# Performance work log

Measured on AMD Instinct MI355X. Metric: run time of the kernel, lower is better.

## Reference

```python
import jax, jax.numpy as jnp
import numpy as np
from itertools import product

SPATIAL1 = (41, 1600, 1408)  # (z,y,x) = grid[::-1] + [1,0,0]
NUM_BATCH = 2
BN_EPS = 1e-3

# ---------- numpy rulebook construction (spconv-style, done once on host) ----------

def _encode(c, shape):
    D, H, W = [int(v) for v in shape]
    return ((c[:, 0].astype(np.int64) * D + c[:, 1]) * H + c[:, 2]) * W + c[:, 3]

def _lookup(skeys, order, cand):
    pos = np.clip(np.searchsorted(skeys, cand), 0, len(skeys) - 1)
    hit = skeys[pos] == cand
    return hit, order[pos]

def _pad_rb(pairs, n_in, n_out):
    P = max(max(len(a) for a, _ in pairs), 1)
    K = len(pairs)
    ii = np.full((K, P), n_in, np.int32)   # sentinel -> zero feature row
    oo = np.full((K, P), n_out, np.int32)  # sentinel -> dummy output row
    for k, (a, b) in enumerate(pairs):
        ii[k, :len(a)] = a
        oo[k, :len(b)] = b
    return ii, oo

def _subm_rb(coords, shape):
    # SubMConv3d k=3 p=1 s=1: output sites == input sites
    N = len(coords)
    keys = _encode(coords, shape)
    order = np.argsort(keys); skeys = keys[order]
    dims = np.array(shape)
    pairs = []
    for off in product((-1, 0, 1), repeat=3):
        nb = coords[:, 1:] + np.array(off)
        ok = (nb >= 0).all(1) & (nb < dims).all(1)
        oid = np.nonzero(ok)[0]
        cand = _encode(np.concatenate([coords[ok, :1], nb[ok]], 1), shape)
        hit, iid = _lookup(skeys, order, cand)
        pairs.append((iid[hit].astype(np.int32), oid[hit].astype(np.int32)))
    return _pad_rb(pairs, N, N)

def _down_rb(coords, in_shape, ks, st, pd):
    # SparseConv3d: output site active iff any kernel tap hits an active input
    dims = np.array(in_shape); ks = np.array(ks); st = np.array(st); pd = np.array(pd)
    out_shape = (dims + 2 * pd - ks) // st + 1
    offs = list(product(*[range(int(k)) for k in ks]))
    outs = []
    for off in offs:
        o = coords[:, 1:] + pd - np.array(off)
        ok = (o % st == 0).all(1)
        od = o // st
        ok &= (od >= 0).all(1) & (od < out_shape).all(1)
        outs.append(np.concatenate([coords[ok, :1], od[ok]], 1))
    out_coords = np.unique(np.concatenate(outs, 0), axis=0)
    keys = _encode(coords, in_shape)
    order = np.argsort(keys); skeys = keys[order]
    pairs = []
    for off in offs:
        ic = out_coords[:, 1:] * st - pd + np.array(off)
        ok = (ic >= 0).all(1) & (ic < dims).all(1)
        oid = np.nonzero(ok)[0]
        cand = _encode(np.concatenate([out_coords[ok, :1], ic[ok]], 1), in_shape)
        hit, iid = _lookup(skeys, order, cand)
        pairs.append((iid[hit].astype(np.int32), oid[hit].astype(np.int32)))
    ii, oo = _pad_rb(pairs, len(coords), len(out_coords))
    return ii, oo, out_coords, tuple(int(v) for v in out_shape)

def _gen_coords(rng):
    # clustered LiDAR-like active voxels (surfaces -> local density)
    D, H, W = SPATIAL1
    per = []
    for b in range(NUM_BATCH):
        centers = rng.integers([3, 30, 30], [D - 4, H - 31, W - 31], size=(600, 3))
        pts = centers[:, None, :] + rng.integers(-3, 4, size=(600, 60, 3))
        pts = np.clip(pts.reshape(-1, 3), 0, np.array([D - 1, H - 1, W - 1]))
        uniq = np.unique(pts, axis=0)
        per.append(np.concatenate([np.full((len(uniq), 1), b, np.int64), uniq], 1))
    return np.concatenate(per, 0)

CHANS = [(27, 4, 16), (27, 16, 16), (27, 16, 32), (27, 32, 32), (27, 32, 32),
         (27, 32, 64), (27, 64, 64), (27, 64, 64), (27, 64, 64), (27, 64, 64),
         (27, 64, 64), (3, 64, 128)]

def setup_inputs() -> dict:
    rng = np.random.default_rng(0)
    coords = _gen_coords(rng)  # (N,4) [b,z,y,x]
    N = len(coords)
    s1i, s1o = _subm_rb(coords, SPATIAL1)
    d2i, d2o, c2, s2 = _down_rb(coords, SPATIAL1, (3, 3, 3), (2, 2, 2), (1, 1, 1))
    s2i, s2o = _subm_rb(c2, s2)
    d3i, d3o, c3, s3 = _down_rb(c2, s2, (3, 3, 3), (2, 2, 2), (1, 1, 1))
    s3i, s3o = _subm_rb(c3, s3)
    d4i, d4o, c4, s4 = _down_rb(c3, s3, (3, 3, 3), (2, 2, 2), (0, 1, 1))
    s4i, s4o = _subm_rb(c4, s4)
    oi, oo, c5, s5 = _down_rb(c4, s4, (3, 1, 1), (2, 1, 1), (0, 0, 0))

    key = jax.random.key(0)
    ks = jax.random.split(key, 40)
    inp = {}
    for i, (K, ci, co) in enumerate(CHANS):
        inp[f"w{i}"] = (jax.random.normal(ks[i], (K, ci, co), jnp.float32)
                         / np.sqrt(K * ci)).astype(jnp.float32)
        kb = jax.random.split(ks[12 + i], 4)
        inp[f"bn{i}"] = jnp.stack([
            jax.random.uniform(kb[0], (co,)) + 0.5,   # gamma
            jax.random.normal(kb[1], (co,)) * 0.1,    # beta
            jax.random.normal(kb[2], (co,)) * 0.1,    # running mean
            jax.random.uniform(kb[3], (co,)) + 0.5,   # running var
        ]).astype(jnp.float32)
    inp["voxels"] = jax.random.normal(ks[30], (N, 5, 4), jnp.float32)
    inp["voxel_num_points"] = jax.random.randint(ks[31], (N,), 0, 6).astype(jnp.int32)
    for name, arr in [("subm1_in", s1i), ("subm1_out", s1o), ("down2_in", d2i),
                      ("down2_out", d2o), ("subm2_in", s2i), ("subm2_out", s2o),
                      ("down3_in", d3i), ("down3_out", d3o), ("subm3_in", s3i),
                      ("subm3_out", s3o), ("down4_in", d4i), ("down4_out", d4o),
                      ("subm4_in", s4i), ("subm4_out", s4o), ("out_in", oi),
                      ("out_out", oo)]:
        inp[name] = jnp.asarray(arr)
    inp["batch_idx"] = jnp.asarray(c5[:, 0].astype(np.int32))
    inp["n2"] = len(c2); inp["n3"] = len(c3); inp["n4"] = len(c4); inp["n5"] = len(c5)
    inp["n_batch"] = NUM_BATCH
    return inp

# ---------- jax forward ----------

def _sconv(feats, w, in_idx, out_idx, n_out):
    # gather -> per-kernel-offset GEMM -> scatter-add (spconv implicit GEMM)
    fpad = jnp.concatenate([feats, jnp.zeros((1, feats.shape[1]), feats.dtype)], 0)
    g = fpad[in_idx]                                  # (K,P,Cin)
    contrib = jnp.einsum('kpi,kio->kpo', g, w)        # (K,P,Cout)
    out = jnp.zeros((n_out + 1, w.shape[2]), feats.dtype)
    return out.at[out_idx].add(contrib)[:n_out]

def _bnrelu(x, bn):
    g, b, m, v = bn  # eval-mode BatchNorm1d, eps=1e-3
    return jax.nn.relu((x - m) * jax.lax.rsqrt(v + BN_EPS) * g + b)

def reference(voxels, voxel_num_points, w0, w1, w2, w3, w4, w5, w6, w7, w8, w9,
              w10, w11, bn0, bn1, bn2, bn3, bn4, bn5, bn6, bn7, bn8, bn9, bn10,
              bn11, subm1_in, subm1_out, down2_in, down2_out, subm2_in, subm2_out,
              down3_in, down3_out, subm3_in, subm3_out, down4_in, down4_out,
              subm4_in, subm4_out, out_in, out_out, batch_idx, n2, n3, n4, n5,
              n_batch):
    # mean-VFE: average point features per voxel
    denom = jnp.maximum(voxel_num_points.astype(voxels.dtype), 1.0)[:, None]
    x = voxels.sum(1) / denom                              # (N,4)
    n1 = x.shape[0]
    x = _bnrelu(_sconv(x, w0, subm1_in, subm1_out, n1), bn0)   # conv_input
    x = _bnrelu(_sconv(x, w1, subm1_in, subm1_out, n1), bn1)   # conv1
    x = _bnrelu(_sconv(x, w2, down2_in, down2_out, n2), bn2)   # conv2 (s2)
    x = _bnrelu(_sconv(x, w3, subm2_in, subm2_out, n2), bn3)
    x = _bnrelu(_sconv(x, w4, subm2_in, subm2_out, n2), bn4)
    x = _bnrelu(_sconv(x, w5, down3_in, down3_out, n3), bn5)   # conv3 (s2)
    x = _bnrelu(_sconv(x, w6, subm3_in, subm3_out, n3), bn6)
    x = _bnrelu(_sconv(x, w7, subm3_in, subm3_out, n3), bn7)
    x = _bnrelu(_sconv(x, w8, down4_in, down4_out, n4), bn8)   # conv4 (s2)
    x = _bnrelu(_sconv(x, w9, subm4_in, subm4_out, n4), bn9)
    x = _bnrelu(_sconv(x, w10, subm4_in, subm4_out, n4), bn10)
    x = _bnrelu(_sconv(x, w11, out_in, out_out, n5), bn11)     # conv_out
    # dc_feats: per-sample global max pool over active voxels (== max_pool1d)
    dc = jax.ops.segment_max(x, batch_idx, num_segments=n_batch)
    return dc
```

## Files before the change

### kernel.cpp

```cpp
#include <hip/hip_runtime.h>

#define TPB 256
typedef unsigned short u16;
typedef __attribute__((ext_vector_type(8))) short short8v;
typedef __attribute__((ext_vector_type(4))) float f32x4;

__device__ __forceinline__ u16 f2bf(float x) {
    unsigned u = __float_as_uint(x);
    return (u16)((u + 0x7FFFu + ((u >> 16) & 1u)) >> 16);
}
__device__ __forceinline__ float bf2f(u16 h) {
    return __uint_as_float(((unsigned)h) << 16);
}

template<int CS>
__device__ __forceinline__ int swzc(int r, int c) {
    constexpr int PH = (CS == 8) ? 0 : 1;
    return c ^ ((r >> PH) & (CS - 1));
}

__device__ __forceinline__ int xcd_swz(int bid, int nwg) {
    int q = nwg >> 3, r = nwg & 7;
    int x = bid & 7, idx = bid >> 3;
    return (x < r ? x * (q + 1) : r * (q + 1) + (x - r) * q) + idx;
}

__device__ __forceinline__ void gld16(const u16* g, u16* l) {
    __builtin_amdgcn_global_load_lds(
        (const __attribute__((address_space(1))) void*)g,
        (__attribute__((address_space(3))) void*)l, 16, 0, 0);
}

__global__ void vfe_kernel(const float* __restrict__ voxels,
                           const int* __restrict__ nump,
                           float* __restrict__ x, int N) {
    int i = blockIdx.x * blockDim.x + threadIdx.x;
    if (i >= N * 4) return;
    int n = i >> 2, c = i & 3;
    const float* v = voxels + (long)n * 20 + c;
    float s = v[0] + v[4] + v[8] + v[12] + v[16];
    x[i] = s / fmaxf((float)nump[n], 1.0f);
}

struct IBE { const int* rin; const int* rout; int* inv; int P, K, n_in, n_out, KP; };
struct IBA { IBE e[8]; };
__global__ void inv_build_all_kernel(IBA a, long grand) {
    long t = (long)blockIdx.x * blockDim.x + threadIdx.x;
    if (t >= grand) return;
    #pragma unroll
    for (int i = 0; i < 8; ++i) {
        if (t < a.e[i].KP) {
            const IBE& E = a.e[i];
            int ii = E.rin[t];
            if (ii != E.n_in) {
                int k = (int)(t / E.P);
                E.inv[(long)k * E.n_out + E.rout[t]] = ii;
            }
            return;
        }
        t -= a.e[i].KP;
    }
}

struct WPE { const float* w; u16* oh; u16* ol; int K, ci, co, total, pci; };
struct WPA { WPE e[11]; };
__global__ void wprep_kernel(WPA a, long grand) {
    long t = (long)blockIdx.x * blockDim.x + threadIdx.x;
    if (t >= grand) return;
    #pragma unroll
    for (int i = 0; i < 11; ++i) {
        if (t < a.e[i].total) {
            const WPE& E = a.e[i];
            if (E.pci) {
                int ci2 = 2 * E.pci;
                int p = (int)(t / (E.co * ci2));
                int rem = (int)(t % (E.co * ci2));
                int o = rem / ci2, ci = rem % ci2;
                int tap = 2 * p + ci / E.pci;
                float x = (tap < 27)
                    ? E.w[((long)tap * E.pci + (ci % E.pci)) * E.co + o] : 0.f;
                u16 h = f2bf(x);
                float lf = x - bf2f(h);
                int cs = ci2 >> 3, ph = (cs == 8) ? 0 : 1;
                int ch = ci >> 3, e = ci & 7;
                int sch = ch ^ ((o >> ph) & (cs - 1));
                long d = ((long)p * E.co + o) * ci2 + sch * 8 + e;
                E.oh[d] = h; E.ol[d] = f2bf(lf);
            } else {
                int cc = E.ci * E.co;
                int k = (int)(t / cc), r = (int)(t % cc), c = r / E.co, o = r % E.co;
                float x = E.w[t];
                u16 h = f2bf(x);
                float lf = x - bf2f(h);
                int cs = E.ci >> 3, ph = (cs == 8) ? 0 : 1;
                int ch = c >> 3, e = c & 7;
                int sch = ch ^ ((o >> ph) & (cs - 1));
                long d = ((long)k * E.co + o) * E.ci + sch * 8 + e;
                E.oh[d] = h; E.ol[d] = f2bf(lf);
            }
            return;
        }
        t -= a.e[i].total;
    }
}

template<int CO, int K>
__global__ __launch_bounds__(256)
void dconv4_kernel(const float* __restrict__ feats,
                   const float* __restrict__ w,
                   const float* __restrict__ bn,
                   const int* __restrict__ inv, int inv_n,
                   u16* __restrict__ oh, u16* __restrict__ ol,
                   int n_out) {
    constexpr int OG = CO / 4;
    __shared__ float sW[K * 4 * CO];
    for (int i = threadIdx.x; i < K * 4 * CO; i += 256) sW[i] = w[i];
    __syncthreads();
    long t = (long)blockIdx.x * 256 + threadIdx.x;
    int row = (int)(t / OG), og = (int)(t % OG);
    if (row >= n_out) return;
    float a0 = 0.f, a1 = 0.f, a2 = 0.f, a3 = 0.f;
    for (int k = 0; k < K; ++k) {
        int idx = inv[(long)k * inv_n + row];
        if (idx < 0) continue;
        float4 av = *(const float4*)(feats + (long)idx * 4);
        const float* wk = sW + k * 4 * CO + og * 4;
        #pragma unroll
        for (int ci = 0; ci < 4; ++ci) {
            float a = (&av.x)[ci];
            a0 = fmaf(a, wk[ci * CO + 0], a0);
            a1 = fmaf(a, wk[ci * CO + 1], a1);
            a2 = fmaf(a, wk[ci * CO + 2], a2);
            a3 = fmaf(a, wk[ci * CO + 3], a3);
        }
    }
    float4 g = *(const float4*)(bn + og * 4);
    float4 b = *(const float4*)(bn + CO + og * 4);
    float4 m = *(const float4*)(bn + 2 * CO + og * 4);
    float4 v = *(const float4*)(bn + 3 * CO + og * 4);
    float o4[4];
    o4[0] = fmaxf((a0 - m.x) * rsqrtf(v.x + 1e-3f) * g.x + b.x, 0.f);
    o4[1] = fmaxf((a1 - m.y) * rsqrtf(v.y + 1e-3f) * g.y + b.y, 0.f);
    o4[2] = fmaxf((a2 - m.z) * rsqrtf(v.z + 1e-3f) * g.z + b.z, 0.f);
    o4[3] = fmaxf((a3 - m.w) * rsqrtf(v.w + 1e-3f) * g.w + b.w, 0.f);
    long base = (long)row * CO + og * 4;
    #pragma unroll
    for (int c = 0; c < 4; ++c) {
        u16 h = f2bf(o4[c]);
        oh[base + c] = h;
        ol[base + c] = f2bf(o4[c] - bf2f(h));
    }
}

template<int CI, int CO, int KPt, int KT, bool PAIRED, int PCI, int EPI>
__global__ __launch_bounds__(256, 4)
void mconv_kernel(const u16* __restrict__ fh, const u16* __restrict__ fl,
                  const u16* __restrict__ wh, const u16* __restrict__ wl,
                  const int* __restrict__ inv,
                  const u16* __restrict__ zpage,
                  float* __restrict__ part, long slab_elems,
                  const float* __restrict__ bn,
                  u16* __restrict__ oh, u16* __restrict__ ol,
                  float* __restrict__ outf,
                  int n_out, int kpb) {
    constexpr int CS  = CI / 8;
    constexpr int LCS = (CS == 8) ? 3 : 2;
    constexpr int PH  = (CS == 8) ? 0 : 1;
    constexpr int KS  = CI / 32;
    constexpr int WC  = (CO >= 32) ? 2 : 1;
    constexpr int MT  = (WC == 2) ? 2 : 1;
    constexpr int NTW = CO / (16 * WC);
    constexpr int ASL = 64 * CS;
    constexpr int BSL = CO * CS;
    constexpr int AIT = (ASL + 255) / 256;
    constexpr int BIT = (BSL + 255) / 256;
    constexpr int SUBCS = PAIRED ? (PCI / 8) : 1;

    __shared__ __align__(16) u16 sAh[64 * CI];
    __shared__ __align__(16) u16 sAl[64 * CI];
    __shared__ __align__(16) u16 sBh[CO * CI];
    __shared__ __align__(16) u16 sBl[CO * CI];

    const int t = threadIdx.x;
    const int bx = xcd_swz(blockIdx.x, gridDim.x);
    const int brow = bx * 64;
    const int kbeg = blockIdx.y * kpb;
    const int kend = (kbeg + kpb < KPt) ? (kbeg + kpb) : KPt;

    const int lane = t & 63, wid = t >> 6;
    const int wr = wid / WC, wc = wid % WC;
    const int frow = lane & 15;
    const int fch  = lane >> 4;

    f32x4 acc[MT][NTW];
    #pragma unroll
    for (int mt = 0; mt < MT; ++mt)
        #pragma unroll
        for (int nt = 0; nt < NTW; ++nt) {
            acc[mt][nt][0] = 0.f; acc[mt][nt][1] = 0.f;
            acc[mt][nt][2] = 0.f; acc[mt][nt][3] = 0.f;
        }

    auto stage = [&](int k) {
        #pragma unroll
        for (int s = 0; s < AIT; ++s) {
            int slot = s * 256 + t;
            if (ASL % 256 == 0 || slot < ASL) {
                int r = slot >> LCS, cc = slot & (CS - 1);
                int c = cc ^ ((r >> PH) & (CS - 1));
                int grow = brow + r;
                const u16 *srcH, *srcL;
                if (PAIRED) {
                    int tap = 2 * k + c / SUBCS;
                    int within = c % SUBCS;
                    int idx = (grow < n_out && tap < KT)
                              ? inv[(long)tap * n_out + grow] : -1;
                    srcH = (idx >= 0) ? fh + (long)idx * PCI + within * 8 : zpage;
                    srcL = (idx >= 0) ? fl + (long)idx * PCI + within * 8 : zpage;
                } else {
                    int idx = (grow < n_out) ? inv[(long)k * n_out + grow] : -1;
                    srcH = (idx >= 0) ? fh + (long)idx * CI + c * 8 : zpage;
                    srcL = (idx >= 0) ? fl + (long)idx * CI + c * 8 : zpage;
                }
                gld16(srcH, sAh + (s * 256 + wid * 64) * 8);
                gld16(srcL, sAl + (s * 256 + wid * 64) * 8);
            }
        }
        const u16* gbh = wh + (long)k * CO * CI;
        const u16* gbl = wl + (long)k * CO * CI;
        #pragma unroll
        for (int s = 0; s < BIT; ++s) {
            int slot = s * 256 + t;
            if (BSL % 256 == 0 || slot < BSL) {
                gld16(gbh + (long)slot * 8, sBh + (s * 256 + wid * 64) * 8);
                gld16(gbl + (long)slot * 8, sBl + (s * 256 + wid * 64) * 8);
            }
        }
    };
    auto compute = [&]() {
        #pragma unroll
        for (int ks = 0; ks < KS; ++ks) {
            int c = ks * 4 + fch;
            short8v ah[MT], al[MT];
            #pragma unroll
            for (int mt = 0; mt < MT; ++mt) {
                int r = wr * (MT * 16) + mt * 16 + frow;
                int o = r * CI + swzc<CS>(r, c) * 8;
                ah[mt] = *(const short8v*)(sAh + o);
                al[mt] = *(const short8v*)(sAl + o);
            }
            #pragma unroll
            for (int nt = 0; nt < NTW; ++nt) {
                int col = wc * (CO / WC) + nt * 16 + frow;
                int o = col * CI + swzc<CS>(col, c) * 8;
                short8v bh = *(const short8v*)(sBh + o);
                short8v bl = *(const short8v*)(sBl + o);
                #pragma unroll
                for (int mt = 0; mt < MT; ++mt) {
                    acc[mt][nt] = __builtin_amdgcn_mfma_f32_16x16x32_bf16(ah[mt], bh, acc[mt][nt], 0, 0, 0);
                    acc[mt][nt] = __builtin_amdgcn_mfma_f32_16x16x32_bf16(ah[mt], bl, acc[mt][nt], 0, 0, 0);
                    acc[mt][nt] = __builtin_amdgcn_mfma_f32_16x16x32_bf16(al[mt], bh, acc[mt][nt], 0, 0, 0);
                }
            }
        }
    };

    for (int k = kbeg; k < kend; ++k) {
        stage(k);
        __syncthreads();
        compute();
        if (k + 1 < kend) __syncthreads();
    }

    if constexpr (EPI == 0) {
        float* dst = part + (long)blockIdx.y * slab_elems;
        #pragma unroll
        for (int mt = 0; mt < MT; ++mt) {
            int orow0 = brow + wr * (MT * 16) + mt * 16 + (lane >> 4) * 4;
            #pragma unroll
            for (int nt = 0; nt < NTW; ++nt) {
                int ocol = wc * (CO / WC) + nt * 16 + (lane & 15);
                #pragma unroll
                for (int j = 0; j < 4; ++j) {
                    int r = orow0 + j;
                    if (r < n_out) dst[(long)r * CO + ocol] = acc[mt][nt][j];
                }
            }
        }
    } else {
        #pragma unroll
        for (int mt = 0; mt < MT; ++mt) {
            int orow0 = brow + wr * (MT * 16) + mt * 16 + (lane >> 4) * 4;
            #pragma unroll
            for (int nt = 0; nt < NTW; ++nt) {
                int ocol = wc * (CO / WC) + nt * 16 + (lane & 15);
                float g = bn[ocol], bb = bn[CO + ocol];
                float m = bn[2 * CO + ocol], vv = bn[3 * CO + ocol];
                float sc = rsqrtf(vv + 1e-3f) * g;
                #pragma unroll
                for (int j = 0; j < 4; ++j) {
                    int r = orow0 + j;
                    if (r < n_out) {
                        float yv = fmaxf((acc[mt][nt][j] - m) * sc + bb, 0.f);
                        if constexpr (EPI == 1) {
                            u16 h = f2bf(yv);
                            oh[(long)r * CO + ocol] = h;
                            ol[(long)r * CO + ocol] = f2bf(yv - bf2f(h));
                        } else {
                            outf[(long)r * CO + ocol] = yv;
                        }
                    }
                }
            }
        }
    }
}

template<bool EMIT16>
__global__ void reduce_bnrelu_kernel(const float* __restrict__ part, long stride,
                                     int ys, const float* __restrict__ bn, int co,
                                     float* __restrict__ outf,
                                     u16* __restrict__ oh, u16* __restrict__ ol,
                                     long total4) {
    long t4 = (long)blockIdx.x * blockDim.x + threadIdx.x;
    if (t4 >= total4) return;
    long base = t4 * 4;
    float4 s = make_float4(0.f, 0.f, 0.f, 0.f);
    for (int y = 0; y < ys; ++y) {
        float4 v = *(const float4*)(part + (long)y * stride + base);
        s.x += v.x; s.y += v.y; s.z += v.z; s.w += v.w;
    }
    int o = (int)(base % co);
    float4 g = *(const float4*)(bn + o);
    float4 b = *(const float4*)(bn + co + o);
    float4 m = *(const float4*)(bn + 2 * co + o);
    float4 v = *(const float4*)(bn + 3 * co + o);
    float y0 = fmaxf((s.x - m.x) * rsqrtf(v.x + 1e-3f) * g.x + b.x, 0.f);
    float y1 = fmaxf((s.y - m.y) * rsqrtf(v.y + 1e-3f) * g.y + b.y, 0.f);
    float y2 = fmaxf((s.z - m.z) * rsqrtf(v.z + 1e-3f) * g.z + b.z, 0.f);
    float y3 = fmaxf((s.w - m.w) * rsqrtf(v.w + 1e-3f) * g.w + b.w, 0.f);
    if (EMIT16) {
        u16 h0 = f2bf(y0), h1 = f2bf(y1), h2 = f2bf(y2), h3 = f2bf(y3);
        ushort4 hv = { h0, h1, h2, h3 };
        ushort4 lv = { f2bf(y0 - bf2f(h0)), f2bf(y1 - bf2f(h1)),
                       f2bf(y2 - bf2f(h2)), f2bf(y3 - bf2f(h3)) };
        *(ushort4*)(oh + base) = hv;
        *(ushort4*)(ol + base) = lv;
    } else {
        *(float4*)(outf + base) = make_float4(y0, y1, y2, y3);
    }
}

__global__ void segmax_kernel(const float* __restrict__ x,
                              const int* __restrict__ bidx,
                              float* __restrict__ out, int rows, int nb) {
    __shared__ float sM[8 * 128];
    for (int i = threadIdx.x; i < nb * 128; i += 256) sM[i] = 0.f;
    __syncthreads();
    int c = threadIdx.x & 127;
    int sub = threadIdx.x >> 7;
    for (int r = blockIdx.x * 2 + sub; r < rows; r += gridDim.x * 2) {
        float v = x[(long)r * 128 + c];
        int b = bidx[r];
        atomicMax((int*)&sM[b * 128 + c], __float_as_int(v));
    }
    __syncthreads();
    for (int i = threadIdx.x; i < nb * 128; i += 256)
        atomicMax((int*)out + i, __float_as_int(sM[i]));
}

extern "C" void kernel_launch(void* const* d_in, const int* in_sizes, int n_in,
                              void* d_out, int out_size, void* d_ws, size_t ws_size,
                              hipStream_t stream) {
    (void)n_in;
    const float* voxels = (const float*)d_in[24];
    const int*   nump   = (const int*)d_in[25];
    const int N  = in_sizes[25];
    const int n2 = in_sizes[30] / 27;
    const int n3 = in_sizes[34] / 27;
    const int n4 = in_sizes[38] / 27;
    const int n5 = in_sizes[42];

    struct L { int wi, rb, K, ci, co, nin, nout; };
    const L layers[12] = {
        {0,  26, 27,  4,  16, N,  N }, {1,  26, 27, 16,  16, N,  N },
        {2,  28, 27, 16,  32, N,  n2}, {3,  30, 27, 32,  32, n2, n2},
        {4,  30, 27, 32,  32, n2, n2}, {5,  32, 27, 32,  64, n2, n3},
        {6,  34, 27, 64,  64, n3, n3}, {7,  34, 27, 64,  64, n3, n3},
        {8,  36, 27, 64,  64, n3, n4}, {9,  38, 27, 64,  64, n4, n4},
        {10, 38, 27, 64,  64, n4, n4}, {11, 40,  3, 64, 128, n4, n5},
    };
    struct RBD { int rb, K, nin, nout; };
    const RBD rbs[8] = {
        {26, 27, N,  N }, {28, 27, N,  n2}, {30, 27, n2, n2}, {32, 27, n2, n3},
        {34, 27, n3, n3}, {36, 27, n3, n4}, {38, 27, n4, n4}, {40, 3,  n4, n5},
    };
    const int invmap[12] = {0, 0, 1, 2, 2, 3, 4, 4, 5, 6, 6, 7};

    size_t feat_elems = (size_t)N * 4, wst_elems = 0, arena_elems = 0;
    size_t wst_off[12];
    for (int i = 0; i < 12; ++i) {
        size_t fe = (size_t)layers[i].nout * layers[i].co;
        if (fe > feat_elems) feat_elems = fe;
        if (i >= 5) { wst_off[i] = wst_elems;
                      wst_elems += (size_t)layers[i].K * layers[i].ci * layers[i].co; }
    }
    for (int r = 0; r < 8; ++r) arena_elems += (size_t)rbs[r].nout * rbs[r].K;
    const int pair_pci[4] = {16, 16, 32, 32};
    const int pair_co[4]  = {16, 32, 32, 32};
    size_t wpd_elems[4], wpd_off[4], wpd_tot = 0;
    for (int j = 0; j < 4; ++j) {
        wpd_elems[j] = (size_t)14 * pair_co[j] * 2 * pair_pci[j];
        wpd_off[j] = wpd_tot; wpd_tot += wpd_elems[j];
    }
    auto al = [](size_t x) { return (x + 255) & ~(size_t)255; };
    char* p = (char*)d_ws;
    u16*   zpage = (u16*)p; p += 256;
    int*   inv_arena = (int*)p; p += al(arena_elems * 4);
    float* bufA = (float*)p; p += al(feat_elems * 4);
    u16* ph[2]; u16* pl[2];
    ph[0] = (u16*)p; p += al(feat_elems * 2);
    pl[0] = (u16*)p; p += al(feat_elems * 2);
    ph[1] = (u16*)p; p += al(feat_elems * 2);
    pl[1] = (u16*)p; p += al(feat_elems * 2);
    u16* wth = (u16*)p; p += al(wst_elems * 2);
    u16* wtl = (u16*)p; p += al(wst_elems * 2);
    u16* wph = (u16*)p; p += al(wpd_tot * 2);
    u16* wpl = (u16*)p; p += al(wpd_tot * 2);
    float* slab = (float*)p;
    size_t slab_budget = ws_size - (size_t)((char*)slab - (char*)d_ws);

    hipMemsetAsync(zpage, 0, 256, stream);

    int* invs[8];
    {
        size_t off = 0;
        for (int r = 0; r < 8; ++r) { invs[r] = inv_arena + off; off += (size_t)rbs[r].nout * rbs[r].K; }
        hipMemsetAsync(inv_arena, 0xFF, arena_elems * sizeof(int), stream);
        IBA ia;
        long grand = 0;
        for (int r = 0; r < 8; ++r) {
            int P  = in_sizes[rbs[r].rb] / rbs[r].K;
            ia.e[r].rin  = (const int*)d_in[rbs[r].rb];
            ia.e[r].rout = (const int*)d_in[rbs[r].rb + 1];
            ia.e[r].inv  = invs[r];
            ia.e[r].P = P; ia.e[r].K = rbs[r].K; ia.e[r].n_in = rbs[r].nin;
            ia.e[r].n_out = rbs[r].nout;
            ia.e[r].KP = rbs[r].K * P;
            grand += ia.e[r].KP;
        }
        inv_build_all_kernel<<<dim3((unsigned)((grand + TPB - 1) / TPB)), dim3(TPB), 0, stream>>>(ia, grand);
    }

    {
        long tot = (long)N * 4;
        vfe_kernel<<<dim3((unsigned)((tot + TPB - 1) / TPB)), dim3(TPB), 0, stream>>>(
            voxels, nump, bufA, N);
    }

    {
        WPA wa;
        long grand = 0;
        for (int i = 5; i < 12; ++i) {
            const L& l = layers[i];
            WPE& E = wa.e[i - 5];
            E.w  = (const float*)d_in[2 * l.wi];
            E.oh = wth + wst_off[i];
            E.ol = wtl + wst_off[i];
            E.K = l.K; E.ci = l.ci; E.co = l.co;
            E.total = l.K * l.ci * l.co;
            E.pci = 0;
            grand += E.total;
        }
        for (int j = 0; j < 4; ++j) {
            WPE& E = wa.e[7 + j];
            E.w  = (const float*)d_in[2 * layers[1 + j].wi];
            E.oh = wph + wpd_off[j];
            E.ol = wpl + wpd_off[j];
            E.K = 27; E.ci = pair_pci[j]; E.co = pair_co[j];
            E.total = (int)wpd_elems[j];
            E.pci = pair_pci[j];
            grand += E.total;
        }
        wprep_kernel<<<dim3((unsigned)((grand + TPB - 1) / TPB)), dim3(TPB), 0, stream>>>(wa, grand);
    }

    {
        const L& l = layers[0];
        long tot = (long)l.nout * 4;
        dconv4_kernel<16, 27><<<dim3((unsigned)((tot + 255) / 256)), 256, 0, stream>>>(
            bufA, (const float*)d_in[0], (const float*)d_in[1], invs[0], l.nout,
            ph[0], pl[0], l.nout);
    }

    int cset = 0;
    for (int i = 1; i < 12; ++i) {
        const L& l = layers[i];
        const int* invp = invs[invmap[i]];
        unsigned blocks = (unsigned)((l.nout + 63) / 64);
        int KPv = (i <= 4) ? 14 : l.K;
        int ysmax = (KPv == 14) ? 9 : ((KPv == 27) ? 27 : 3);
        size_t per = (size_t)l.nout * l.co * 4;
        int ys = 1;
        while (ys < ysmax && blocks * (unsigned)ys < 768) ys *= 3;
        if (ys > ysmax) ys = ysmax;
        while (ys > 1 && (size_t)ys * per > slab_budget) ys /= 3;
        int kpb = (KPv + ys - 1) / ys;
        long slab_elems = (long)l.nout * l.co;
        dim3 grid(blocks, (unsigned)ys);
        const float* bn = (const float*)d_in[2 * l.wi + 1];
        const u16* fh = ph[cset];
        const u16* fl = pl[cset];
        const u16* whp = (i >= 5) ? wth + wst_off[i] : wph + wpd_off[i - 1];
        const u16* wlp = (i >= 5) ? wtl + wst_off[i] : wpl + wpd_off[i - 1];

        #define MCONV(CI_, CO_, KP_, KT_, PRD_, PCI_)                                  \
            do {                                                                       \
                if (ys == 1 && i < 11)                                                 \
                    mconv_kernel<CI_, CO_, KP_, KT_, PRD_, PCI_, 1><<<grid, 256, 0, stream>>>( \
                        fh, fl, whp, wlp, invp, zpage, nullptr, 0, bn,                 \
                        ph[cset ^ 1], pl[cset ^ 1], nullptr, l.nout, kpb);             \
                else if (ys == 1)                                                      \
                    mconv_kernel<CI_, CO_, KP_, KT_, PRD_, PCI_, 2><<<grid, 256, 0, stream>>>( \
                        fh, fl, whp, wlp, invp, zpage, nullptr, 0, bn,                 \
                        nullptr, nullptr, bufA, l.nout, kpb);                          \
                else                                                                   \
                    mconv_kernel<CI_, CO_, KP_, KT_, PRD_, PCI_, 0><<<grid, 256, 0, stream>>>( \
                        fh, fl, whp, wlp, invp, zpage, slab, slab_elems, bn,           \
                        nullptr, nullptr, nullptr, l.nout, kpb);                       \
            } while (0)

        switch (i) {
        case 1:          MCONV(32, 16, 14, 27, true, 16);  break;
        case 2:          MCONV(32, 32, 14, 27, true, 16);  break;
        case 3: case 4:  MCONV(64, 32, 14, 27, true, 32);  break;
        case 5:          MCONV(32, 64, 27, 27, false, 32); break;
        case 11:         MCONV(64, 128, 3, 3, false, 64);  break;
        default:         MCONV(64, 64, 27, 27, false, 64); break;
        }
        #undef MCONV

        if (ys == 1) {
            if (i < 11) cset ^= 1;
        } else {
            long total4 = ((long)l.nout * l.co) / 4;
            unsigned rblocks = (unsigned)((total4 + TPB - 1) / TPB);
            if (i < 11) {
                reduce_bnrelu_kernel<true><<<dim3(rblocks), dim3(TPB), 0, stream>>>(
                    slab, slab_elems, ys, bn, l.co,
                    nullptr, ph[cset ^ 1], pl[cset ^ 1], total4);
                cset ^= 1;
            } else {
                reduce_bnrelu_kernel<false><<<dim3(rblocks), dim3(TPB), 0, stream>>>(
                    slab, slab_elems, ys, bn, l.co, bufA, nullptr, nullptr, total4);
            }
        }
    }

    hipMemsetAsync(d_out, 0, (size_t)out_size * sizeof(float), stream);
    const int* bidx = (const int*)d_in[42];
    int nb = out_size / 128;
    segmax_kernel<<<dim3(128), dim3(256), 0, stream>>>(bufA, bidx, (float*)d_out, n5, nb);
}
```

Measured before the change: 390.0 us.

## Load gathered features and weights directly into registers, drop LDS staging

```diff
diff --git a/kernel.cpp b/kernel.cpp
--- a/kernel.cpp
+++ b/kernel.cpp
@@ -23,12 +23,6 @@
     int q = nwg >> 3, r = nwg & 7;
     int x = bid & 7, idx = bid >> 3;
     return (x < r ? x * (q + 1) : r * (q + 1) + (x - r) * q) + idx;
-}
-
-__device__ __forceinline__ void gld16(const u16* g, u16* l) {
-    __builtin_amdgcn_global_load_lds(
-        (const __attribute__((address_space(1))) void*)g,
-        (__attribute__((address_space(3))) void*)l, 16, 0, 0);
 }
 
 __global__ void vfe_kernel(const float* __restrict__ voxels,
@@ -164,22 +158,11 @@
                   float* __restrict__ outf,
                   int n_out, int kpb) {
     constexpr int CS  = CI / 8;
-    constexpr int LCS = (CS == 8) ? 3 : 2;
-    constexpr int PH  = (CS == 8) ? 0 : 1;
     constexpr int KS  = CI / 32;
     constexpr int WC  = (CO >= 32) ? 2 : 1;
     constexpr int MT  = (WC == 2) ? 2 : 1;
     constexpr int NTW = CO / (16 * WC);
-    constexpr int ASL = 64 * CS;
-    constexpr int BSL = CO * CS;
-    constexpr int AIT = (ASL + 255) / 256;
-    constexpr int BIT = (BSL + 255) / 256;
     constexpr int SUBCS = PAIRED ? (PCI / 8) : 1;
-
-    __shared__ __align__(16) u16 sAh[64 * CI];
-    __shared__ __align__(16) u16 sAl[64 * CI];
-    __shared__ __align__(16) u16 sBh[CO * CI];
-    __shared__ __align__(16) u16 sBl[CO * CI];
 
     const int t = threadIdx.x;
     const int bx = xcd_swz(blockIdx.x, gridDim.x);
@@ -191,6 +174,14 @@
     const int wr = wid / WC, wc = wid % WC;
     const int frow = lane & 15;
     const int fch  = lane >> 4;
+
+    int  row[MT];
+    bool rv[MT];
+    #pragma unroll
+    for (int mt = 0; mt < MT; ++mt) {
+        row[mt] = brow + wr * (MT * 16) + mt * 16 + frow;
+        rv[mt]  = row[mt] < n_out;
+    }
 
     f32x4 acc[MT][NTW];
     #pragma unroll
@@ -201,60 +192,43 @@
             acc[mt][nt][2] = 0.f; acc[mt][nt][3] = 0.f;
         }
 
-    auto stage = [&](int k) {
-        #pragma unroll
-        for (int s = 0; s < AIT; ++s) {
-            int slot = s * 256 + t;
-            if (ASL % 256 == 0 || slot < ASL) {
-                int r = slot >> LCS, cc = slot & (CS - 1);
-                int c = cc ^ ((r >> PH) & (CS - 1));
-                int grow = brow + r;
-                const u16 *srcH, *srcL;
-                if (PAIRED) {
-                    int tap = 2 * k + c / SUBCS;
-                    int within = c % SUBCS;
-                    int idx = (grow < n_out && tap < KT)
-                              ? inv[(long)tap * n_out + grow] : -1;
-                    srcH = (idx >= 0) ? fh + (long)idx * PCI + within * 8 : zpage;
-                    srcL = (idx >= 0) ? fl + (long)idx * PCI + within * 8 : zpage;
-                } else {
-                    int idx = (grow < n_out) ? inv[(long)k * n_out + grow] : -1;
-                    srcH = (idx >= 0) ? fh + (long)idx * CI + c * 8 : zpage;
-                    srcL = (idx >= 0) ? fl + (long)idx * CI + c * 8 : zpage;
-                }
-                gld16(srcH, sAh + (s * 256 + wid * 64) * 8);
-                gld16(srcL, sAl + (s * 256 + wid * 64) * 8);
-            }
-        }
-        const u16* gbh = wh + (long)k * CO * CI;
-        const u16* gbl = wl + (long)k * CO * CI;
-        #pragma unroll
-        for (int s = 0; s < BIT; ++s) {
-            int slot = s * 256 + t;
-            if (BSL % 256 == 0 || slot < BSL) {
-                gld16(gbh + (long)slot * 8, sBh + (s * 256 + wid * 64) * 8);
-                gld16(gbl + (long)slot * 8, sBl + (s * 256 + wid * 64) * 8);
-            }
-        }
-    };
-    auto compute = [&]() {
+    for (int k = kbeg; k < kend; ++k) {
+        const u16* wbh = wh + (long)k * CO * CI;
+        const u16* wbl = wl + (long)k * CO * CI;
+        int idxk[MT];
+        if (!PAIRED) {
+            #pragma unroll
+            for (int mt = 0; mt < MT; ++mt)
+                idxk[mt] = rv[mt] ? inv[(long)k * n_out + row[mt]] : -1;
+        }
         #pragma unroll
         for (int ks = 0; ks < KS; ++ks) {
             int c = ks * 4 + fch;
             short8v ah[MT], al[MT];
             #pragma unroll
             for (int mt = 0; mt < MT; ++mt) {
-                int r = wr * (MT * 16) + mt * 16 + frow;
-                int o = r * CI + swzc<CS>(r, c) * 8;
-                ah[mt] = *(const short8v*)(sAh + o);
-                al[mt] = *(const short8v*)(sAl + o);
+                const u16 *sH, *sL;
+                if (PAIRED) {
+                    int tap = 2 * k + c / SUBCS;
+                    int within = c % SUBCS;
+                    int idx = (rv[mt] && tap < KT)
+                              ? inv[(long)tap * n_out + row[mt]] : -1;
+                    sH = (idx >= 0) ? fh + (long)idx * PCI + within * 8 : zpage;
+                    sL = (idx >= 0) ? fl + (long)idx * PCI + within * 8 : zpage;
+                } else {
+                    int idx = idxk[mt];
+                    sH = (idx >= 0) ? fh + (long)idx * CI + c * 8 : zpage;
+                    sL = (idx >= 0) ? fl + (long)idx * CI + c * 8 : zpage;
+                }
+                ah[mt] = *(const short8v*)sH;
+                al[mt] = *(const short8v*)sL;
             }
             #pragma unroll
             for (int nt = 0; nt < NTW; ++nt) {
                 int col = wc * (CO / WC) + nt * 16 + frow;
                 int o = col * CI + swzc<CS>(col, c) * 8;
-                short8v bh = *(const short8v*)(sBh + o);
-                short8v bl = *(const short8v*)(sBl + o);
+                short8v bh = *(const short8v*)(wbh + o);
+                short8v bl = *(const short8v*)(wbl + o);
                 #pragma unroll
                 for (int mt = 0; mt < MT; ++mt) {
                     acc[mt][nt] = __builtin_amdgcn_mfma_f32_16x16x32_bf16(ah[mt], bh, acc[mt][nt], 0, 0, 0);
@@ -263,13 +237,6 @@
                 }
             }
         }
-    };
-
-    for (int k = kbeg; k < kend; ++k) {
-        stage(k);
-        __syncthreads();
-        compute();
-        if (k + 1 < kend) __syncthreads();
     }
 
     if constexpr (EPI == 0) {
```

Measured after the change: 530.4 us. 1.36x slower.
